# Optimization experiments

Measured on AMD Instinct MI355X. Metric: run time of the kernel, lower is better.

Reference implementation:

```python
import jax, jax.numpy as jnp
import numpy as np

LIGAND_W = 1.0
SIDECHAIN_W = 0.5
LIGAND_DIST_W = 0.2
SIDECHAIN_DIST_W = 0.1
CUTOFF = 5.0
EPS = 1e-12


def _pdist(x):
    # x: [..., N, 3] -> (dist [..., N, N], sq [..., N, N]); safe sqrt for grads
    d = x[..., :, None, :] - x[..., None, :, :]
    sq = jnp.sum(d * d, axis=-1)
    return jnp.sqrt(jnp.maximum(sq, EPS)), sq


def _masked_dist_loss(pred, tgt, valid):
    # pred/tgt: [..., N, 3], valid: [..., N] float. Returns (per-group loss, has-any flag)
    pd, _ = _pdist(pred)
    td, tsq = _pdist(tgt)
    pair = valid[..., :, None] * valid[..., None, :]
    dmask = pair * (tsq > 0.0).astype(pred.dtype) * (td <= CUTOFF).astype(pred.dtype)
    num = jnp.sum(dmask * (pd - td) ** 2, axis=(-1, -2))
    den = jnp.sum(dmask, axis=(-1, -2))
    return num / jnp.maximum(den, 1.0), den > 0.0


def setup_inputs() -> dict:
    key = jax.random.key(0)
    k1, k2, k3, k4, k5, k6 = jax.random.split(key, 6)
    B, L, R, A = 64, 512, 1024, 14
    ligand_tgt = jax.random.normal(k2, (B, L, 3), dtype=jnp.float32) * 3.0
    ligand_pred = ligand_tgt + 0.5 * jax.random.normal(k1, (B, L, 3), dtype=jnp.float32)
    sidechain_tgt = jax.random.normal(k4, (B, R, A, 3), dtype=jnp.float32) * 2.0
    sidechain_pred = sidechain_tgt + 0.5 * jax.random.normal(k3, (B, R, A, 3), dtype=jnp.float32)
    ligand_mask = jax.random.bernoulli(k5, 0.9, (B, L))
    atom_mask = jax.random.bernoulli(k6, 0.7, (B, R, A))
    return {
        'ligand_pred': ligand_pred, 'ligand_tgt': ligand_tgt,
        'sidechain_pred': sidechain_pred, 'sidechain_tgt': sidechain_tgt,
        'ligand_mask': ligand_mask, 'atom_mask': atom_mask,
    }


def reference(ligand_pred, ligand_tgt, sidechain_pred, sidechain_tgt, ligand_mask, atom_mask):
    f = ligand_pred.dtype
    lm = ligand_mask.astype(f)              # [B, L]
    am = atom_mask.astype(f)                # [B, R, A]

    # --- ligand coord loss: per-batch mse (mean over valid atoms * 3), then mean over batches ---
    se = jnp.sum((ligand_pred - ligand_tgt) ** 2, axis=-1) * lm   # [B, L]
    lig_cnt = jnp.sum(lm, axis=-1)                                # [B]
    ligand_loss = jnp.mean(jnp.sum(se, axis=-1) / (3.0 * jnp.maximum(lig_cnt, 1.0)))

    # --- ligand distance-preservation loss ---
    lig_d, lig_has = _masked_dist_loss(ligand_pred, ligand_tgt, lm)  # [B], [B]
    ligand_dist_loss = jnp.sum(jnp.where(lig_has, lig_d, 0.0)) / jnp.maximum(jnp.sum(lig_has.astype(f)), 1.0)

    # --- sidechain coord loss: per-atom mse (mean over 3), mean over all valid atoms ---
    atom_mse = jnp.mean((sidechain_pred - sidechain_tgt) ** 2, axis=-1)  # [B, R, A]
    sc_cnt = jnp.sum(am)
    sidechain_loss = jnp.sum(atom_mse * am) / jnp.maximum(sc_cnt, 1.0)

    # --- sidechain distance-preservation loss: per-residue groups ---
    sc_d, sc_has = _masked_dist_loss(sidechain_pred, sidechain_tgt, am)  # [B, R]
    sidechain_dist_loss = jnp.sum(jnp.where(sc_has, sc_d, 0.0)) / jnp.maximum(jnp.sum(sc_has.astype(f)), 1.0)

    total = (LIGAND_W * ligand_loss
             + LIGAND_DIST_W * ligand_dist_loss
             + SIDECHAIN_W * sidechain_loss
             + SIDECHAIN_DIST_W * sidechain_dist_loss)
    return total
```

## Files before the change

### kernel.cpp

```cpp
#include <hip/hip_runtime.h>

#define CUTOFF 5.0f
#define DEPS 1e-12f
#define FSQRT(x) __builtin_amdgcn_sqrtf(x)


#define NSC_BLK 512
#define NLIG_BLK 512
#define GRID (NSC_BLK + NLIG_BLK)

#define PAIR_EVAL(ti, pi, tjx, tjy, tjz, pjx, pjy, pjz, w, numv, denv)    \
  {                                                                       \
    float dx = (ti).x - (tjx), dy = (ti).y - (tjy), dz = (ti).z - (tjz);  \
    float tsq = dx * dx + dy * dy + dz * dz;                              \
    float td = FSQRT(fmaxf(tsq, DEPS));                                   \
    float ww = (w);                                                       \
    ww = (tsq > 0.f) ? ww : 0.f;                                          \
    ww = (td <= CUTOFF) ? ww : 0.f;                                       \
    float qx = (pi).x - (pjx), qy = (pi).y - (pjy), qz = (pi).z - (pjz);  \
    float pd = FSQRT(fmaxf(qx * qx + qy * qy + qz * qz, DEPS));           \
    float dd = pd - td;                                                   \
    numv += ww * dd * dd;                                                 \
    denv += ww;                                                           \
  }

__global__ __launch_bounds__(256) void fused_kernel(
    const float* __restrict__ lig_pred, const float* __restrict__ lig_tgt,
    const int* __restrict__ lig_mask,
    const float* __restrict__ sc_pred, const float* __restrict__ sc_tgt,
    const int* __restrict__ sc_mask,
    float* __restrict__ ws) {
  const int tid = threadIdx.x;
  __shared__ float4 stage4[1344];
  __shared__ float red[4][4];

  if (blockIdx.x < NSC_BLK) {
    const int sb = blockIdx.x;
    float ax[7], ay[7], az[7];
    float bx[7], by[7], bz[7];
    float m[7];

    const float4* srcp = (const float4*)(sc_pred + (size_t)sb * 5376);
    for (int k = tid; k < 1344; k += 256) stage4[k] = srcp[k];
    __syncthreads();
    {
      const float* s = ((const float*)stage4) + tid * 21;
#pragma unroll
      for (int a = 0; a < 7; a++) { ax[a] = s[3 * a]; ay[a] = s[3 * a + 1]; az[a] = s[3 * a + 2]; }
    }
    __syncthreads();
    const float4* srct = (const float4*)(sc_tgt + (size_t)sb * 5376);
    for (int k = tid; k < 1344; k += 256) stage4[k] = srct[k];
    __syncthreads();
    {
      const float* s = ((const float*)stage4) + tid * 21;
#pragma unroll
      for (int a = 0; a < 7; a++) { bx[a] = s[3 * a]; by[a] = s[3 * a + 1]; bz[a] = s[3 * a + 2]; }
    }
    const int* mp = sc_mask + (size_t)sb * 1792 + tid * 7;
#pragma unroll
    for (int a = 0; a < 7; a++) m[a] = (mp[a] != 0) ? 1.f : 0.f;

    float mse = 0.f, am = 0.f;
#pragma unroll
    for (int a = 0; a < 7; a++) {
      float dx = ax[a] - bx[a], dy = ay[a] - by[a], dz = az[a] - bz[a];
      mse += m[a] * ((dx * dx + dy * dy + dz * dz) * (1.f / 3.f));
      am += m[a];
    }

    float num = 0.f, den = 0.f;
#pragma unroll
    for (int js = 0; js < 7; js++) {
#pragma unroll
      for (int side = 0; side < 2; side++) {
        float jx, jy, jz, kx, ky, kz, mj;
        if (side == 0) {
          jx = ax[js]; jy = ay[js]; jz = az[js];
          kx = bx[js]; ky = by[js]; kz = bz[js];
          mj = m[js];
        } else {
          jx = __shfl_xor(ax[js], 1, 64); jy = __shfl_xor(ay[js], 1, 64);
          jz = __shfl_xor(az[js], 1, 64);
          kx = __shfl_xor(bx[js], 1, 64); ky = __shfl_xor(by[js], 1, 64);
          kz = __shfl_xor(bz[js], 1, 64);
          mj = __shfl_xor(m[js], 1, 64);
        }
#pragma unroll
        for (int i = 0; i < 7; i++) {
          float dx = bx[i] - kx, dy = by[i] - ky, dz = bz[i] - kz;
          float tsq = dx * dx + dy * dy + dz * dz;
          float td = FSQRT(fmaxf(tsq, DEPS));
          float w = m[i] * mj;
          w = (tsq > 0.f) ? w : 0.f;
          w = (td <= CUTOFF) ? w : 0.f;
          float qx = ax[i] - jx, qy = ay[i] - jy, qz = az[i] - jz;
          float pd = FSQRT(fmaxf(qx * qx + qy * qy + qz * qz, DEPS));
          float d = pd - td;
          num += w * d * d;
          den += w;
        }
      }
    }
    float num_g = num + __shfl_xor(num, 1, 64);
    float den_g = den + __shfl_xor(den, 1, 64);
    float val = (den_g > 0.f) ? 0.5f * (num_g / fmaxf(den_g, 1.f)) : 0.f;
    float has = (den_g > 0.f) ? 0.5f : 0.f;

    for (int off = 32; off > 0; off >>= 1) {
      mse += __shfl_down(mse, off, 64);
      am += __shfl_down(am, off, 64);
      val += __shfl_down(val, off, 64);
      has += __shfl_down(has, off, 64);
    }
    int lane = tid & 63, wv = tid >> 6;
    if (lane == 0) { red[0][wv] = mse; red[1][wv] = am; red[2][wv] = val; red[3][wv] = has; }
    __syncthreads();
    if (tid == 0) {
      float* p = ws + 1088 + (size_t)sb * 4;
      p[0] = red[0][0] + red[0][1] + red[0][2] + red[0][3];
      p[1] = red[1][0] + red[1][1] + red[1][2] + red[1][3];
      p[2] = red[2][0] + red[2][1] + red[2][2] + red[2][3];
      p[3] = red[3][0] + red[3][1] + red[3][2] + red[3][3];
    }
  } else {
    const int L = 512;
    const int lb = blockIdx.x - NSC_BLK;
    const int b = lb >> 3;
    const int t = lb & 7;
    const int i0a = 32 * t;
    const int i0b = 32 * (15 - t);
    const float* pb = lig_pred + (size_t)b * L * 3;
    const float* tb = lig_tgt + (size_t)b * L * 3;
    const int* mb = lig_mask + (size_t)b * L;

    float4* st4 = stage4;
    float4* sp4 = stage4 + 64;

    if (tid < 128) {
      int which = tid >> 5;
      int idx = tid & 31;
      int i = ((which & 1) ? i0b : i0a) + idx;
      if (which < 2) {
        st4[(which << 5) + idx] =
            make_float4(tb[3 * i], tb[3 * i + 1], tb[3 * i + 2], (mb[i] != 0) ? 1.f : 0.f);
      } else {
        sp4[((which & 1) << 5) + idx] =
            make_float4(pb[3 * i], pb[3 * i + 1], pb[3 * i + 2], 0.f);
      }
    }

    const int jA0 = i0a + tid;
    const int jA1r = i0a + 256 + tid;
    const int jA1 = jA1r & (L - 1);
    const int jBr = i0b + tid;
    const int jB = jBr & (L - 1);

    float pA0x = pb[3 * jA0], pA0y = pb[3 * jA0 + 1], pA0z = pb[3 * jA0 + 2];
    float tA0x = tb[3 * jA0], tA0y = tb[3 * jA0 + 1], tA0z = tb[3 * jA0 + 2];
    float mA0 = (mb[jA0] != 0) ? 1.f : 0.f;
    float pA1x = pb[3 * jA1], pA1y = pb[3 * jA1 + 1], pA1z = pb[3 * jA1 + 2];
    float tA1x = tb[3 * jA1], tA1y = tb[3 * jA1 + 1], tA1z = tb[3 * jA1 + 2];
    float mA1 = (jA1r < L && mb[jA1] != 0) ? 1.f : 0.f;
    float pBx = pb[3 * jB], pBy = pb[3 * jB + 1], pBz = pb[3 * jB + 2];
    float tBx = tb[3 * jB], tBy = tb[3 * jB + 1], tBz = tb[3 * jB + 2];
    float mB = (jBr < L && mb[jB] != 0) ? 1.f : 0.f;

    float se = 0.f, cnt = 0.f;
    if (t == 0) {
      float dx = pA0x - tA0x, dy = pA0y - tA0y, dz = pA0z - tA0z;
      se += mA0 * (dx * dx + dy * dy + dz * dz);
      cnt += mA0;
      dx = pA1x - tA1x; dy = pA1y - tA1y; dz = pA1z - tA1z;
      se += mA1 * (dx * dx + dy * dy + dz * dz);
      cnt += mA1;
    }
    __syncthreads();

    float nA0 = 0.f, dA0 = 0.f, nA1 = 0.f, dA1 = 0.f, nB = 0.f, dB = 0.f;
#pragma unroll 8
    for (int ii = 0; ii < 32; ii++) {
      float4 tiA = st4[ii];
      float4 piA = sp4[ii];
      float4 tiB = st4[32 + ii];
      float4 piB = sp4[32 + ii];
      float wA0 = (tid > ii) ? tiA.w * mA0 : 0.f;
      PAIR_EVAL(tiA, piA, tA0x, tA0y, tA0z, pA0x, pA0y, pA0z, wA0, nA0, dA0);
      float wA1 = tiA.w * mA1;
      PAIR_EVAL(tiA, piA, tA1x, tA1y, tA1z, pA1x, pA1y, pA1z, wA1, nA1, dA1);
      float wB = (tid > ii) ? tiB.w * mB : 0.f;
      PAIR_EVAL(tiB, piB, tBx, tBy, tBz, pBx, pBy, pBz, wB, nB, dB);
    }

    float num = nA0 + nA1 + nB, den = dA0 + dA1 + dB;
    for (int off = 32; off > 0; off >>= 1) {
      num += __shfl_down(num, off, 64);
      den += __shfl_down(den, off, 64);
      se += __shfl_down(se, off, 64);
      cnt += __shfl_down(cnt, off, 64);
    }
    int lane = tid & 63, wv = tid >> 6;
    if (lane == 0) { red[0][wv] = num; red[1][wv] = den; red[2][wv] = se; red[3][wv] = cnt; }
    __syncthreads();
    if (tid == 0) {
      ws[lb * 2 + 0] = red[0][0] + red[0][1] + red[0][2] + red[0][3];
      ws[lb * 2 + 1] = red[1][0] + red[1][1] + red[1][2] + red[1][3];
      if (t == 0) {
        float se_t = red[2][0] + red[2][1] + red[2][2] + red[2][3];
        float cnt_t = red[3][0] + red[3][1] + red[3][2] + red[3][3];
        ws[1024 + b] = se_t / (3.f * fmaxf(cnt_t, 1.f));
      }
    }
  }
}

__global__ __launch_bounds__(256) void finalize_kernel(const float* __restrict__ ws,
                                                       float* __restrict__ out) {
  const int tid = threadIdx.x;
  __shared__ float sred[4][4];

  const float* sc = ws + 1088;
  float s0 = 0.f, s1 = 0.f, s2 = 0.f, s3 = 0.f;
  for (int i = tid; i < 512; i += 256) {
    s0 += sc[4 * i + 0]; s1 += sc[4 * i + 1]; s2 += sc[4 * i + 2]; s3 += sc[4 * i + 3];
  }
  for (int off = 32; off > 0; off >>= 1) {
    s0 += __shfl_down(s0, off, 64);
    s1 += __shfl_down(s1, off, 64);
    s2 += __shfl_down(s2, off, 64);
    s3 += __shfl_down(s3, off, 64);
  }
  int lane = tid & 63, wv = tid >> 6;
  if (lane == 0) { sred[0][wv] = s0; sred[1][wv] = s1; sred[2][wv] = s2; sred[3][wv] = s3; }
  __syncthreads();

  float lval = 0.f, lhas = 0.f, lcoord = 0.f;
  if (tid < 64) {
    float n = 0.f, d = 0.f;
    for (int t = 0; t < 8; t++) {
      n += ws[(tid * 8 + t) * 2 + 0];
      d += ws[(tid * 8 + t) * 2 + 1];
    }
    lval = (d > 0.f) ? n / fmaxf(d, 1.f) : 0.f;
    lhas = (d > 0.f) ? 1.f : 0.f;
    lcoord = ws[1024 + tid];
    for (int off = 32; off > 0; off >>= 1) {
      lval += __shfl_down(lval, off, 64);
      lhas += __shfl_down(lhas, off, 64);
      lcoord += __shfl_down(lcoord, off, 64);
    }
  }
  if (tid == 0) {
    float sc_mse = sred[0][0] + sred[0][1] + sred[0][2] + sred[0][3];
    float sc_am = sred[1][0] + sred[1][1] + sred[1][2] + sred[1][3];
    float sc_val = sred[2][0] + sred[2][1] + sred[2][2] + sred[2][3];
    float sc_has = sred[3][0] + sred[3][1] + sred[3][2] + sred[3][3];
    float ligand_loss = lcoord * (1.f / 64.f);
    float ligand_dist_loss = lval / fmaxf(lhas, 1.f);
    float sidechain_loss = sc_mse / fmaxf(sc_am, 1.f);
    float sidechain_dist_loss = sc_val / fmaxf(sc_has, 1.f);
    out[0] = ligand_loss + 0.2f * ligand_dist_loss + 0.5f * sidechain_loss +
             0.1f * sidechain_dist_loss;
  }
}

extern "C" void kernel_launch(void* const* d_in, const int* in_sizes, int n_in,
                              void* d_out, int out_size, void* d_ws, size_t ws_size,
                              hipStream_t stream) {
  const float* ligand_pred = (const float*)d_in[0];
  const float* ligand_tgt = (const float*)d_in[1];
  const float* sidechain_pred = (const float*)d_in[2];
  const float* sidechain_tgt = (const float*)d_in[3];
  const int* ligand_mask = (const int*)d_in[4];
  const int* atom_mask = (const int*)d_in[5];
  float* out = (float*)d_out;
  float* ws = (float*)d_ws;

  fused_kernel<<<GRID, 256, 0, stream>>>(ligand_pred, ligand_tgt, ligand_mask,
                                         sidechain_pred, sidechain_tgt, atom_mask, ws);
  finalize_kernel<<<1, 256, 0, stream>>>(ws, out);
}
```

Baseline: 105.8 us.

## Assign one residue per thread and compute only the upper-triangle sidechain pairs

The sidechain path changes from two threads per residue, which shuffled atoms between lanes and evaluated all ordered pairs, to one thread per residue holding all 14 atoms in registers. Only the i<j pairs are evaluated, and the sums are doubled to stand in for the symmetric half. Masked target atoms are pushed far away so the distance cutoff removes them, which drops the mask multiplies, the tsq>0 test and the epsilon clamps. The number of sidechain blocks is halved and the finalize reduction shrinks to match. The far-away offset trick and the removed tsq>0 check assume that no two valid target atoms coincide and that the offsets never fall inside the cutoff. Register pressure per thread also rises.

```diff
diff --git a/kernel.cpp b/kernel.cpp
--- a/kernel.cpp
+++ b/kernel.cpp
@@ -1,11 +1,10 @@
 #include <hip/hip_runtime.h>
 
 #define CUTOFF 5.0f
-#define DEPS 1e-12f
 #define FSQRT(x) __builtin_amdgcn_sqrtf(x)
 
 
-#define NSC_BLK 512
+#define NSC_BLK 256
 #define NLIG_BLK 512
 #define GRID (NSC_BLK + NLIG_BLK)
 
@@ -13,14 +12,13 @@
   {                                                                       \
     float dx = (ti).x - (tjx), dy = (ti).y - (tjy), dz = (ti).z - (tjz);  \
     float tsq = dx * dx + dy * dy + dz * dz;                              \
-    float td = FSQRT(fmaxf(tsq, DEPS));                                   \
+    float td = FSQRT(tsq);                                                \
     float ww = (w);                                                       \
-    ww = (tsq > 0.f) ? ww : 0.f;                                          \
     ww = (td <= CUTOFF) ? ww : 0.f;                                       \
     float qx = (pi).x - (pjx), qy = (pi).y - (pjy), qz = (pi).z - (pjz);  \
-    float pd = FSQRT(fmaxf(qx * qx + qy * qy + qz * qz, DEPS));           \
+    float pd = FSQRT(qx * qx + qy * qy + qz * qz);                        \
     float dd = pd - td;                                                   \
-    numv += ww * dd * dd;                                                 \
+    numv += (ww * dd) * dd;                                               \
     denv += ww;                                                           \
   }
 
@@ -36,76 +34,76 @@
 
   if (blockIdx.x < NSC_BLK) {
     const int sb = blockIdx.x;
-    float ax[7], ay[7], az[7];
-    float bx[7], by[7], bz[7];
-    float m[7];
-
-    const float4* srcp = (const float4*)(sc_pred + (size_t)sb * 5376);
-    for (int k = tid; k < 1344; k += 256) stage4[k] = srcp[k];
-    __syncthreads();
-    {
-      const float* s = ((const float*)stage4) + tid * 21;
-#pragma unroll
-      for (int a = 0; a < 7; a++) { ax[a] = s[3 * a]; ay[a] = s[3 * a + 1]; az[a] = s[3 * a + 2]; }
-    }
-    __syncthreads();
-    const float4* srct = (const float4*)(sc_tgt + (size_t)sb * 5376);
-    for (int k = tid; k < 1344; k += 256) stage4[k] = srct[k];
-    __syncthreads();
-    {
-      const float* s = ((const float*)stage4) + tid * 21;
-#pragma unroll
-      for (int a = 0; a < 7; a++) { bx[a] = s[3 * a]; by[a] = s[3 * a + 1]; bz[a] = s[3 * a + 2]; }
-    }
-    const int* mp = sc_mask + (size_t)sb * 1792 + tid * 7;
-#pragma unroll
-    for (int a = 0; a < 7; a++) m[a] = (mp[a] != 0) ? 1.f : 0.f;
+    const int rl = tid & 127;
+    const int rh = tid >> 7;
+    float ax[14], ay[14], az[14];
+    float bx[14], by[14], bz[14];
+
+    const float4* srcp = (const float4*)(sc_pred + (size_t)sb * 10752);
+    const float4* srct = (const float4*)(sc_tgt + (size_t)sb * 10752);
+#pragma unroll
+    for (int h = 0; h < 2; h++) {
+      if (h) __syncthreads();
+      for (int k = tid; k < 1344; k += 256) stage4[k] = srcp[h * 1344 + k];
+      __syncthreads();
+      if (rh == h) {
+        const float* s = ((const float*)stage4) + rl * 42;
+#pragma unroll
+        for (int a = 0; a < 14; a++) {
+          ax[a] = s[3 * a]; ay[a] = s[3 * a + 1]; az[a] = s[3 * a + 2];
+        }
+      }
+    }
+#pragma unroll
+    for (int h = 0; h < 2; h++) {
+      __syncthreads();
+      for (int k = tid; k < 1344; k += 256) stage4[k] = srct[h * 1344 + k];
+      __syncthreads();
+      if (rh == h) {
+        const float* s = ((const float*)stage4) + rl * 42;
+#pragma unroll
+        for (int a = 0; a < 14; a++) {
+          bx[a] = s[3 * a]; by[a] = s[3 * a + 1]; bz[a] = s[3 * a + 2];
+        }
+      }
+    }
+
+    const int2* mp2 = (const int2*)(sc_mask + ((size_t)sb * 256 + tid) * 14);
+    float m[14];
+#pragma unroll
+    for (int k = 0; k < 7; k++) {
+      int2 v = mp2[k];
+      m[2 * k] = (v.x != 0) ? 1.f : 0.f;
+      m[2 * k + 1] = (v.y != 0) ? 1.f : 0.f;
+    }
 
     float mse = 0.f, am = 0.f;
 #pragma unroll
-    for (int a = 0; a < 7; a++) {
+    for (int a = 0; a < 14; a++) {
       float dx = ax[a] - bx[a], dy = ay[a] - by[a], dz = az[a] - bz[a];
       mse += m[a] * ((dx * dx + dy * dy + dz * dz) * (1.f / 3.f));
       am += m[a];
+      bx[a] += (1.f - m[a]) * (30000.f * (float)(a + 1));
     }
 
     float num = 0.f, den = 0.f;
 #pragma unroll
-    for (int js = 0; js < 7; js++) {
-#pragma unroll
-      for (int side = 0; side < 2; side++) {
-        float jx, jy, jz, kx, ky, kz, mj;
-        if (side == 0) {
-          jx = ax[js]; jy = ay[js]; jz = az[js];
-          kx = bx[js]; ky = by[js]; kz = bz[js];
-          mj = m[js];
-        } else {
-          jx = __shfl_xor(ax[js], 1, 64); jy = __shfl_xor(ay[js], 1, 64);
-          jz = __shfl_xor(az[js], 1, 64);
-          kx = __shfl_xor(bx[js], 1, 64); ky = __shfl_xor(by[js], 1, 64);
-          kz = __shfl_xor(bz[js], 1, 64);
-          mj = __shfl_xor(m[js], 1, 64);
-        }
-#pragma unroll
-        for (int i = 0; i < 7; i++) {
-          float dx = bx[i] - kx, dy = by[i] - ky, dz = bz[i] - kz;
-          float tsq = dx * dx + dy * dy + dz * dz;
-          float td = FSQRT(fmaxf(tsq, DEPS));
-          float w = m[i] * mj;
-          w = (tsq > 0.f) ? w : 0.f;
-          w = (td <= CUTOFF) ? w : 0.f;
-          float qx = ax[i] - jx, qy = ay[i] - jy, qz = az[i] - jz;
-          float pd = FSQRT(fmaxf(qx * qx + qy * qy + qz * qz, DEPS));
-          float d = pd - td;
-          num += w * d * d;
-          den += w;
-        }
-      }
-    }
-    float num_g = num + __shfl_xor(num, 1, 64);
-    float den_g = den + __shfl_xor(den, 1, 64);
-    float val = (den_g > 0.f) ? 0.5f * (num_g / fmaxf(den_g, 1.f)) : 0.f;
-    float has = (den_g > 0.f) ? 0.5f : 0.f;
+    for (int j = 1; j < 14; j++) {
+#pragma unroll
+      for (int i = 0; i < j; i++) {
+        float dx = bx[i] - bx[j], dy = by[i] - by[j], dz = bz[i] - bz[j];
+        float tsq = dx * dx + dy * dy + dz * dz;
+        float td = FSQRT(tsq);
+        float w = (td <= CUTOFF) ? 1.f : 0.f;
+        float qx = ax[i] - ax[j], qy = ay[i] - ay[j], qz = az[i] - az[j];
+        float pd = FSQRT(qx * qx + qy * qy + qz * qz);
+        float d = pd - td;
+        num += (w * d) * d;
+        den += w;
+      }
+    }
+    float val = (den > 0.f) ? (num + num) / fmaxf(den + den, 1.f) : 0.f;
+    float has = (den > 0.f) ? 1.f : 0.f;
 
     for (int off = 32; off > 0; off >>= 1) {
       mse += __shfl_down(mse, off, 64);
@@ -219,11 +217,8 @@
   const int tid = threadIdx.x;
   __shared__ float sred[4][4];
 
-  const float* sc = ws + 1088;
-  float s0 = 0.f, s1 = 0.f, s2 = 0.f, s3 = 0.f;
-  for (int i = tid; i < 512; i += 256) {
-    s0 += sc[4 * i + 0]; s1 += sc[4 * i + 1]; s2 += sc[4 * i + 2]; s3 += sc[4 * i + 3];
-  }
+  const float* sc = ws + 1088 + (size_t)tid * 4;
+  float s0 = sc[0], s1 = sc[1], s2 = sc[2], s3 = sc[3];
   for (int off = 32; off > 0; off >>= 1) {
     s0 += __shfl_down(s0, off, 64);
     s1 += __shfl_down(s1, off, 64);
```

After: 106.2 us. No clear change (+0.4%).
